# Kernel tuning notes

Measured on AMD Instinct MI355X. Metric: run time of the kernel, lower is better.

Reference implementation:

```python
import jax, jax.numpy as jnp
import numpy as np

NUM_CLASSES = 13
HIDDEN = 64
NUM_LAYERS = 2
NODE_FEAT = 1 + 4 + NUM_CLASSES  # 18
N_NODES = 100000
N_EDGES = 1600000


def _glorot(key, shape):
    fan_in, fan_out = shape[0], shape[1]
    lim = (6.0 / (fan_in + fan_out)) ** 0.5
    return jax.random.uniform(key, shape, jnp.float32, -lim, lim)


def setup_inputs() -> dict:
    key = jax.random.key(0)
    ks = jax.random.split(key, 32)
    H = HIDDEN
    inp = {
        "node_features": jax.random.normal(ks[0], (N_NODES, NODE_FEAT), jnp.float32),
        "edge_index": jax.random.randint(ks[1], (2, N_EDGES), 0, N_NODES, jnp.int32),
        "edge_weights": jax.random.uniform(ks[2], (N_EDGES,), jnp.float32),
        "embed_W": _glorot(ks[3], (NODE_FEAT, H)),
        "embed_b": jnp.zeros((H,), jnp.float32),
        # stacked per-layer params, leading dim = NUM_LAYERS
        "msg_W1": jnp.stack([_glorot(ks[4 + i], (2 * H, H)) for i in range(NUM_LAYERS)]),
        "msg_b1": jnp.zeros((NUM_LAYERS, H), jnp.float32),
        "msg_W2": jnp.stack([_glorot(ks[8 + i], (H, H)) for i in range(NUM_LAYERS)]),
        "msg_b2": jnp.zeros((NUM_LAYERS, H), jnp.float32),
        "att_W1": jnp.stack([_glorot(ks[12 + i], (2 * H, H // 2)) for i in range(NUM_LAYERS)]),
        "att_b1": jnp.zeros((NUM_LAYERS, H // 2), jnp.float32),
        "att_W2": jnp.stack([_glorot(ks[16 + i], (H // 2, 1)) for i in range(NUM_LAYERS)]),
        "att_b2": jnp.zeros((NUM_LAYERS, 1), jnp.float32),
        "upd_W1": jnp.stack([_glorot(ks[20 + i], (2 * H, H)) for i in range(NUM_LAYERS)]),
        "upd_b1": jnp.zeros((NUM_LAYERS, H), jnp.float32),
        "upd_W2": jnp.stack([_glorot(ks[24 + i], (H, H)) for i in range(NUM_LAYERS)]),
        "upd_b2": jnp.zeros((NUM_LAYERS, H), jnp.float32),
        "head_W": _glorot(ks[28], (H, 1)),
        "head_b": jnp.zeros((1,), jnp.float32),
    }
    return inp


def _mlp2(x, W1, b1, W2, b2):
    return jax.nn.relu(x @ W1 + b1) @ W2 + b2


def reference(node_features, edge_index, edge_weights,
              embed_W, embed_b,
              msg_W1, msg_b1, msg_W2, msg_b2,
              att_W1, att_b1, att_W2, att_b2,
              upd_W1, upd_b1, upd_W2, upd_b2,
              head_W, head_b):
    row, col = edge_index[0], edge_index[1]
    x = jax.nn.relu(node_features @ embed_W + embed_b)  # [N, H]
    num_nodes = x.shape[0]
    for l in range(NUM_LAYERS):
        cat = jnp.concatenate([x[row], x[col]], axis=-1)  # [E, 2H]
        messages = _mlp2(cat, msg_W1[l], msg_b1[l], msg_W2[l], msg_b2[l])  # [E, H]
        att = jax.nn.sigmoid(_mlp2(cat, att_W1[l], att_b1[l], att_W2[l], att_b2[l])[:, 0])  # [E]
        fw = edge_weights * att
        messages = messages * fw[:, None]
        aggregated = jax.ops.segment_sum(messages, col, num_segments=num_nodes)  # [N, H]
        norm = jax.ops.segment_sum(fw, col, num_segments=num_nodes)
        norm = jnp.clip(norm, 1e-6, None)
        aggregated = aggregated / norm[:, None]
        x_new = _mlp2(jnp.concatenate([x, aggregated], axis=-1),
                      upd_W1[l], upd_b1[l], upd_W2[l], upd_b2[l])
        x = jax.nn.relu(x_new + x)
    series_repr = jnp.max(x, axis=0)  # [H]
    binary_logit = (series_repr @ head_W + head_b)[0]
    return binary_logit
```

## Files before the change

### kernel.cpp

```cpp
#include <hip/hip_runtime.h>
#include <hip/hip_bf16.h>
#include <math.h>

#define H 64
#define F 18
#define NPW 16
#define NBKT 1024
#define EPB 8192

typedef _Float16 f16x8 __attribute__((ext_vector_type(8)));
typedef _Float16 f16x4 __attribute__((ext_vector_type(4)));
typedef float f32x4 __attribute__((ext_vector_type(4)));

__global__ __launch_bounds__(256) void embed_kernel(
    const float* __restrict__ nf, const float* __restrict__ W,
    const float* __restrict__ b, _Float16* __restrict__ xh, int N)
{
    int n = blockIdx.x * 256 + threadIdx.x;
    if (n >= N) return;
    float acc[H];
#pragma unroll
    for (int j = 0; j < H; ++j) acc[j] = b[j];
    const float* f = nf + (long)n * F;
#pragma unroll
    for (int i = 0; i < F; ++i) {
        float c = f[i];
        const float* w = W + i * H;
#pragma unroll
        for (int j = 0; j < H; ++j) acc[j] += c * w[j];
    }
    union { uint4 v[8]; _Float16 h[64]; } O;
#pragma unroll
    for (int j = 0; j < H; ++j) O.h[j] = (_Float16)fmaxf(acc[j], 0.f);
    uint4* xo = (uint4*)(xh + (size_t)n * H);
#pragma unroll
    for (int i = 0; i < 8; ++i) xo[i] = O.v[i];
}

__global__ __launch_bounds__(256) void packfrag_uv_kernel(
    const float* __restrict__ mW1, const float* __restrict__ aW1,
    f16x8* __restrict__ uvB)
{
    int t = blockIdx.x * 256 + threadIdx.x;
    if (t >= 3072) return;
    int lane = t & 63;
    int frag = t >> 6;
    int l = frag / 24, rem = frag % 24;
    int side = rem / 12, q = rem % 12;
    int nt = q >> 1, kk = q & 1;
    int quad = lane >> 4, l15 = lane & 15;
    int col = nt * 16 + l15;
    f16x8 v;
#pragma unroll
    for (int j = 0; j < 8; ++j) {
        int k = side * 64 + kk * 32 + quad * 8 + j;
        float w = (col < 64) ? mW1[(size_t)l * 8192 + k * 64 + col]
                             : aW1[(size_t)l * 4096 + k * 32 + (col - 64)];
        v[j] = (_Float16)w;
    }
    uvB[(size_t)frag * 64 + lane] = v;
}

__global__ __launch_bounds__(256) void prep_update_kernel(
    const float* __restrict__ mW2, const float* __restrict__ mb2,
    const float* __restrict__ uW1,
    float* __restrict__ M2U, float* __restrict__ mbu)
{
    int t = blockIdx.x * 256 + threadIdx.x;
    if (t >= 2 * 64 * 64) return;
    int l = t >> 12, r = t & 4095;
    int i = r >> 6, j = r & 63;
    const float* W2 = mW2 + (size_t)l * 4096;
    const float* U1b = uW1 + (size_t)l * 8192 + 4096;
    float s = 0.f;
    for (int k = 0; k < 64; ++k) s += W2[i * 64 + k] * U1b[k * 64 + j];
    M2U[t] = s;
    if (i == 0) {
        float sb = 0.f;
        const float* b2 = mb2 + (size_t)l * 64;
        for (int k = 0; k < 64; ++k) sb += b2[k] * U1b[k * 64 + j];
        mbu[l * 64 + j] = sb;
    }
}

__global__ __launch_bounds__(256) void packfrag_upd_kernel(
    const float* __restrict__ uW1, const float* __restrict__ M2U,
    const float* __restrict__ uW2, f16x8* __restrict__ updB)
{
    int t = blockIdx.x * 256 + threadIdx.x;
    if (t >= 3072) return;
    int lane = t & 63;
    int frag = t >> 6;
    int l = frag / 24, f = frag % 24;
    int quad = lane >> 4, l15 = lane & 15;
    int g = f >> 3, ff = f & 7;
    int nt = ff >> 1, kk = ff & 1;
    const float* src;
    if (g == 0)      src = uW1 + (size_t)l * 8192;
    else if (g == 1) src = M2U + (size_t)l * 4096;
    else             src = uW2 + (size_t)l * 4096;
    f16x8 v;
#pragma unroll
    for (int j = 0; j < 8; ++j) {
        int k = kk * 32 + quad * 8 + j;
        v[j] = (_Float16)src[k * 64 + nt * 16 + l15];
    }
    updB[(size_t)frag * 64 + lane] = v;
}

__global__ __launch_bounds__(256) void scan1_kernel(
    const int* __restrict__ deg, int* __restrict__ part,
    int* __restrict__ bsum, int N)
{
    __shared__ int lds[256];
    int t = threadIdx.x;
    int base = blockIdx.x * 1024 + t * 4;
    int v[4];
#pragma unroll
    for (int s = 0; s < 4; ++s) v[s] = (base + s < N) ? deg[base + s] : 0;
    int sum = v[0] + v[1] + v[2] + v[3];
    lds[t] = sum;
    __syncthreads();
    for (int off = 1; off < 256; off <<= 1) {
        int xv = (t >= off) ? lds[t - off] : 0;
        __syncthreads();
        lds[t] += xv;
        __syncthreads();
    }
    int excl = lds[t] - sum;
    if (t == 255) bsum[blockIdx.x] = lds[255];
    int p = excl;
#pragma unroll
    for (int s = 0; s < 4; ++s) {
        if (base + s < N) part[base + s] = p;
        p += v[s];
    }
}

__global__ __launch_bounds__(256) void scan2_kernel(int* __restrict__ bsum, int nb)
{
    __shared__ int lds[256];
    int t = threadIdx.x;
    int v = (t < nb) ? bsum[t] : 0;
    lds[t] = v;
    __syncthreads();
    for (int off = 1; off < 256; off <<= 1) {
        int xv = (t >= off) ? lds[t - off] : 0;
        __syncthreads();
        lds[t] += xv;
        __syncthreads();
    }
    if (t < nb) bsum[t] = lds[t] - v;
}

__global__ __launch_bounds__(256) void scan3_kernel(
    int* __restrict__ part, const int* __restrict__ bsum, int N)
{
    int i = blockIdx.x * 256 + threadIdx.x;
    if (i >= N) return;
    part[i] = part[i] + bsum[i >> 10];
}

__global__ __launch_bounds__(256) void count_bucket_kernel(
    const int* __restrict__ col, int* __restrict__ cnt,
    int E, int NB, int NBK, int BS)
{
    __shared__ int lc[NBKT];
    int t = threadIdx.x;
    for (int i = t; i < NBK; i += 256) lc[i] = 0;
    __syncthreads();
    for (int s = 0; s < EPB / 256; ++s) {
        int e = blockIdx.x * EPB + s * 256 + t;
        if (e < E) atomicAdd(lc + (unsigned)col[e] / (unsigned)BS, 1);
    }
    __syncthreads();
    for (int i = t; i < NBK; i += 256)
        cnt[(size_t)i * NB + blockIdx.x] = lc[i];
}

__global__ __launch_bounds__(256) void place_kernel(
    const int* __restrict__ row, const int* __restrict__ col,
    const float* __restrict__ ew, const int* __restrict__ off,
    int2* __restrict__ edata, int E, int NB, int NBK, int BS)
{
    __shared__ int lc[NBKT];
    int t = threadIdx.x;
    for (int i = t; i < NBK; i += 256) lc[i] = 0;
    __syncthreads();
    for (int s = 0; s < EPB / 256; ++s) {
        int e = blockIdx.x * EPB + s * 256 + t;
        if (e < E) {
            int cv = col[e];
            int c = (unsigned)cv / (unsigned)BS;
            int lcol = cv - c * BS;
            int r = atomicAdd(lc + c, 1);
            int pos = off[(size_t)c * NB + blockIdx.x] + r;
            edata[pos] = make_int2(row[e] | (lcol << 20), __float_as_int(ew[e]));
        }
    }
}

__global__ __launch_bounds__(256) void bucket_sort_kernel(
    int2* __restrict__ edata, const int* __restrict__ off,
    int* __restrict__ deg, int* __restrict__ startp,
    int NB, int BS, int N, int E, int NBK)
{
    __shared__ int hist[256];
    __shared__ int psum[256];
    int b = blockIdx.x;
    int t = threadIdx.x;
    int base = off[(size_t)b * NB];
    int end  = (b + 1 < NBK) ? off[(size_t)(b + 1) * NB] : E;
    int cnt = end - base;
    int nlo = b * BS;

    hist[t] = 0;
    __syncthreads();

    int2 regs[8];
    int lnode[8];
#pragma unroll
    for (int ii = 0; ii < 8; ++ii) {
        int i = t + ii * 256;
        if (i < cnt) {
            regs[ii] = edata[base + i];
            lnode[ii] = ((unsigned)regs[ii].x) >> 20;
            atomicAdd(hist + lnode[ii], 1);
        }
    }
    __syncthreads();

    int cv = hist[t];
    psum[t] = cv;
    __syncthreads();
    for (int o = 1; o < 256; o <<= 1) {
        int xv = (t >= o) ? psum[t - o] : 0;
        __syncthreads();
        psum[t] += xv;
        __syncthreads();
    }
    int excl = psum[t] - cv;
    int ng = nlo + t;
    if (t < BS && ng < N) {
        deg[ng] = cv;
        startp[ng] = base + excl;
    }
    hist[t] = excl;
    __syncthreads();

#pragma unroll
    for (int ii = 0; ii < 8; ++ii) {
        int i = t + ii * 256;
        if (i < cnt) {
            int pos = atomicAdd(hist + lnode[ii], 1);
            edata[base + pos] = make_int2(regs[ii].x & 0xFFFFF, regs[ii].y);
        }
    }
}

__global__ __launch_bounds__(256) void uv_mfma_kernel(
    const _Float16* __restrict__ xh, const f16x8* __restrict__ Bf,
    const float* __restrict__ mb1, const float* __restrict__ ab1,
    _Float16* __restrict__ UV, int N, int nbside)
{
    int bid = blockIdx.x;
    int side = (bid >= nbside) ? 1 : 0;
    int b = bid - side * nbside;
    int lane = threadIdx.x & 63;
    int wid = (b * 256 + (int)threadIdx.x) >> 6;
    int quad = lane >> 4, l15 = lane & 15;
    int nbase = wid * 64;
    if (nbase >= N) return;

    const f16x8* Bs = Bf + side * 12 * 64;
    f16x8 B[12];
#pragma unroll
    for (int i = 0; i < 12; ++i) B[i] = Bs[i * 64 + lane];
    float bv[6];
#pragma unroll
    for (int nt = 0; nt < 6; ++nt) {
        int col = nt * 16 + l15;
        bv[nt] = side ? 0.f : (col < 64 ? mb1[col] : ab1[col - 64]);
    }

    for (int mt = 0; mt < 4; ++mt) {
        int na = nbase + mt * 16 + l15;
        if (na >= N) na = N - 1;
        const f16x8* xrow = (const f16x8*)(xh + (size_t)na * H);
        f16x8 Ax[2];
        Ax[0] = xrow[quad];
        Ax[1] = xrow[4 + quad];

        f32x4 C[6];
#pragma unroll
        for (int nt = 0; nt < 6; ++nt) {
            f32x4 cc = {bv[nt], bv[nt], bv[nt], bv[nt]};
#pragma unroll
            for (int kk = 0; kk < 2; ++kk)
                cc = __builtin_amdgcn_mfma_f32_16x16x32_f16(Ax[kk], B[nt * 2 + kk], cc, 0, 0, 0);
            C[nt] = cc;
        }
#pragma unroll
        for (int r = 0; r < 4; ++r) {
            int n = nbase + mt * 16 + quad * 4 + r;
            if (n < N) {
#pragma unroll
                for (int nt = 0; nt < 6; ++nt)
                    UV[(size_t)n * 192 + side * 96 + nt * 16 + l15] = (_Float16)C[nt][r];
            }
        }
    }
}

__global__ __launch_bounds__(256) void edge_gather_kernel(
    const _Float16* __restrict__ UV,
    const int2* __restrict__ edata,
    const int* __restrict__ startp, const int* __restrict__ deg,
    const float* __restrict__ aW2, const float* __restrict__ ab2,
    _Float16* __restrict__ aggN, float* __restrict__ snorm, int N)
{
    int wid = (blockIdx.x * 256 + threadIdx.x) >> 6;
    int lane = threadIdx.x & 63;
    int g = lane >> 3, s = lane & 7;
    int n0 = wid * NPW;
    if (n0 >= N) return;
    int n1 = n0 + NPW; if (n1 > N) n1 = N;

    float aw2v[4];
#pragma unroll
    for (int j = 0; j < 4; ++j) aw2v[j] = aW2[s * 4 + j];
    float ab2v = ab2[0];

    for (int n = n0; n < n1; ++n) {
        int e0 = startp[n];
        int d = deg[n];
        int iters = (d + 7) >> 3;
        const _Float16* vrow = UV + (size_t)n * 192 + 96;
        f16x8 vm = *(const f16x8*)(vrow + s * 8);
        f16x4 va = *(const f16x4*)(vrow + 64 + s * 4);

        float acc[8];
#pragma unroll
        for (int j = 0; j < 8; ++j) acc[j] = 0.f;
        float rfw = 0.f;

        if (iters > 0) {
            int2 ed0, ed1 = {0, 0}, ed2 = {0, 0};
            f16x8 um0;
            f16x4 ua0;
            {
                int ei = g;
                ed0 = edata[e0 + (ei < d ? ei : 0)];
                const _Float16* ur = UV + (size_t)ed0.x * 192;
                um0 = *(const f16x8*)(ur + s * 8);
                ua0 = *(const f16x4*)(ur + 64 + s * 4);
            }
            if (iters > 1) {
                int ei = 8 + g;
                ed1 = edata[e0 + (ei < d ? ei : 0)];
            }
            for (int it = 0; it < iters; ++it) {
                f16x8 umn = um0;
                f16x4 uan = ua0;
                if (it + 1 < iters) {
                    const _Float16* ur = UV + (size_t)ed1.x * 192;
                    umn = *(const f16x8*)(ur + s * 8);
                    uan = *(const f16x4*)(ur + 64 + s * 4);
                }
                if (it + 2 < iters) {
                    int ei = (it + 2) * 8 + g;
                    ed2 = edata[e0 + (ei < d ? ei : 0)];
                }

                int ei = it * 8 + g;
                float ew = (ei < d) ? __int_as_float(ed0.y) : 0.f;
                float pp = 0.f;
#pragma unroll
                for (int j = 0; j < 4; ++j) {
                    _Float16 za = ua0[j] + va[j];
                    za = za > (_Float16)0 ? za : (_Float16)0;
                    pp += (float)za * aw2v[j];
                }
                pp += __shfl_xor(pp, 1);
                pp += __shfl_xor(pp, 2);
                pp += __shfl_xor(pp, 4);
                float fw = ew / (1.f + __expf(-(pp + ab2v)));
#pragma unroll
                for (int j = 0; j < 8; ++j) {
                    _Float16 z = um0[j] + vm[j];
                    z = z > (_Float16)0 ? z : (_Float16)0;
                    acc[j] += (float)z * fw;
                }
                rfw += fw;

                ed0 = ed1; ed1 = ed2; um0 = umn; ua0 = uan;
            }
        }

#pragma unroll
        for (int o = 8; o <= 32; o <<= 1) {
#pragma unroll
            for (int j = 0; j < 8; ++j) acc[j] += __shfl_xor(acc[j], o);
            rfw += __shfl_xor(rfw, o);
        }
        float inv = 1.f / fmaxf(rfw, 1e-6f);
        if (g == 0) {
            union { _Float16 h[8]; uint4 v; } O;
#pragma unroll
            for (int j = 0; j < 8; ++j) O.h[j] = (_Float16)(acc[j] * inv);
            *(uint4*)(aggN + (size_t)n * H + s * 8) = O.v;
        }
        if (lane == 0) snorm[n] = rfw * inv;
    }
}

__global__ __launch_bounds__(256, 2) void update_mfma_kernel(
    _Float16* __restrict__ xh, const _Float16* __restrict__ agg,
    const float* __restrict__ snorm,
    const f16x8* __restrict__ Bfrag,
    const float* __restrict__ mbu,
    const float* __restrict__ ub1, const float* __restrict__ ub2, int N)
{
    __shared__ __align__(16) _Float16 hlds[4][16 * 80];
    int wib = threadIdx.x >> 6;
    int lane = threadIdx.x & 63;
    int wid = (blockIdx.x * 256 + threadIdx.x) >> 6;
    int quad = lane >> 4, l15 = lane & 15;
    int nbase = wid * 64;
    if (nbase >= N) return;

    f16x8 Bu[8], Bm[8], Bw[8];
#pragma unroll
    for (int i = 0; i < 8; ++i) {
        Bu[i] = Bfrag[i * 64 + lane];
        Bm[i] = Bfrag[(8 + i) * 64 + lane];
        Bw[i] = Bfrag[(16 + i) * 64 + lane];
    }
    float mbuv[4], b1v[4], b2v[4];
#pragma unroll
    for (int nt = 0; nt < 4; ++nt) {
        mbuv[nt] = mbu[nt * 16 + l15];
        b1v[nt] = ub1[nt * 16 + l15];
        b2v[nt] = ub2[nt * 16 + l15];
    }

    for (int mt = 0; mt < 4; ++mt) {
        int na = nbase + mt * 16 + l15;
        if (na >= N) na = N - 1;
        const f16x8* xrow = (const f16x8*)(xh + (size_t)na * H);
        f16x8 Ax[2];
        Ax[0] = xrow[quad];
        Ax[1] = xrow[4 + quad];
        const f16x8* arow = (const f16x8*)(agg + (size_t)na * H);
        f16x8 Aa[2];
        Aa[0] = arow[quad];
        Aa[1] = arow[4 + quad];

        f32x4 Cx[4], Ca[4];
#pragma unroll
        for (int nt = 0; nt < 4; ++nt) {
            f32x4 cx = {0.f, 0.f, 0.f, 0.f}, ca = {0.f, 0.f, 0.f, 0.f};
#pragma unroll
            for (int kk = 0; kk < 2; ++kk) {
                cx = __builtin_amdgcn_mfma_f32_16x16x32_f16(Ax[kk], Bu[nt * 2 + kk], cx, 0, 0, 0);
                ca = __builtin_amdgcn_mfma_f32_16x16x32_f16(Aa[kk], Bm[nt * 2 + kk], ca, 0, 0, 0);
            }
            Cx[nt] = cx; Ca[nt] = ca;
        }

        int noder = nbase + mt * 16 + quad * 4;
        float sn_r[4];
#pragma unroll
        for (int r = 0; r < 4; ++r) {
            int ng = noder + r; if (ng >= N) ng = N - 1;
            sn_r[r] = snorm[ng];
        }

#pragma unroll
        for (int nt = 0; nt < 4; ++nt) {
#pragma unroll
            for (int r = 0; r < 4; ++r) {
                float hv = fmaxf(Cx[nt][r] + Ca[nt][r]
                                 + sn_r[r] * mbuv[nt] + b1v[nt], 0.f);
                hlds[wib][(quad * 4 + r) * 80 + nt * 16 + l15] = (_Float16)hv;
            }
        }
        __asm__ __volatile__("s_waitcnt lgkmcnt(0)" ::: "memory");
        f16x8 Ah[2];
        Ah[0] = *(const f16x8*)&hlds[wib][l15 * 80 + quad * 8];
        Ah[1] = *(const f16x8*)&hlds[wib][l15 * 80 + 32 + quad * 8];
        __asm__ __volatile__("s_waitcnt lgkmcnt(0)" ::: "memory");

        f32x4 C2[4];
#pragma unroll
        for (int nt = 0; nt < 4; ++nt) {
            f32x4 cc = {0.f, 0.f, 0.f, 0.f};
#pragma unroll
            for (int kk = 0; kk < 2; ++kk)
                cc = __builtin_amdgcn_mfma_f32_16x16x32_f16(Ah[kk], Bw[nt * 2 + kk], cc, 0, 0, 0);
            C2[nt] = cc;
        }

#pragma unroll
        for (int r = 0; r < 4; ++r) {
            int ng = noder + r;
            if (ng < N) {
#pragma unroll
                for (int nt = 0; nt < 4; ++nt) {
                    size_t idx = (size_t)ng * H + nt * 16 + l15;
                    float xo = (float)xh[idx];
                    xh[idx] = (_Float16)fmaxf(C2[nt][r] + b2v[nt] + xo, 0.f);
                }
            }
        }
    }
}

__global__ __launch_bounds__(256) void max_kernel(
    const _Float16* __restrict__ xh16, unsigned int* __restrict__ serp, int N)
{
    int j = threadIdx.x & (H - 1);
    int g = (blockIdx.x * 256 + threadIdx.x) >> 6;
    int stride = (gridDim.x * 256) >> 6;
    float m = 0.f;
    for (int n = g; n < N; n += stride)
        m = fmaxf(m, (float)xh16[(size_t)n * H + j]);
    atomicMax(serp + j, __float_as_uint(m));
}

__global__ void head_kernel(const unsigned int* __restrict__ serp,
                            const float* __restrict__ hW,
                            const float* __restrict__ hb,
                            float* __restrict__ out)
{
    int j = threadIdx.x;
    float v = __uint_as_float(serp[j]) * hW[j];
#pragma unroll
    for (int off = 32; off > 0; off >>= 1) v += __shfl_down(v, off);
    if (j == 0) out[0] = v + hb[0];
}

extern "C" void kernel_launch(void* const* d_in, const int* in_sizes, int n_in,
                              void* d_out, int out_size, void* d_ws, size_t ws_size,
                              hipStream_t stream)
{
    const float* nf  = (const float*)d_in[0];
    const int*   ei  = (const int*)d_in[1];
    const float* ew  = (const float*)d_in[2];
    const float* eW  = (const float*)d_in[3];
    const float* eb_ = (const float*)d_in[4];
    const float* mW1 = (const float*)d_in[5];
    const float* mb1 = (const float*)d_in[6];
    const float* mW2 = (const float*)d_in[7];
    const float* mb2 = (const float*)d_in[8];
    const float* aW1 = (const float*)d_in[9];
    const float* ab1 = (const float*)d_in[10];
    const float* aW2 = (const float*)d_in[11];
    const float* ab2 = (const float*)d_in[12];
    const float* uW1 = (const float*)d_in[13];
    const float* ub1 = (const float*)d_in[14];
    const float* uW2 = (const float*)d_in[15];
    const float* ub2 = (const float*)d_in[16];
    const float* hW  = (const float*)d_in[17];
    const float* hb  = (const float*)d_in[18];

    int N = in_sizes[0] / F;
    int E = in_sizes[2];
    const int* row = ei;
    const int* col = ei + E;

    size_t Nr = ((size_t)N + 3) & ~(size_t)3;
    size_t Er = ((size_t)E + 3) & ~(size_t)3;

    int BS  = (N + NBKT - 1) / NBKT;
    int NBK = (N + BS - 1) / BS;
    int NB  = (E + EPB - 1) / EPB;
    size_t M  = (size_t)NBK * NB;
    size_t Mr = (M + 3) & ~(size_t)3;

    _Float16* xh   = (_Float16*)d_ws;
    _Float16* aggN = xh + Nr * 64;
    float* snorm   = (float*)(aggN + Nr * 64);
    unsigned int* serp = (unsigned int*)(snorm + Nr);
    int* deg       = (int*)(serp + 64);
    int* startp    = deg + Nr;
    int* bsum      = startp + Nr;
    float* M2U     = (float*)(bsum + 256);
    float* mbu     = M2U + 8192;
    f16x8* updB    = (f16x8*)(mbu + 128);
    f16x8* uvB     = updB + 3072;
    _Float16* UV   = (_Float16*)(uvB + 3072);
    int* cnt       = (int*)(UV + Nr * 192);
    int* off       = cnt + Mr;
    int2* edata    = (int2*)(off + Mr);

    int nb_n = (N + 255) / 256;
    int nbA = (int)((M + 1023) / 1024);

    count_bucket_kernel<<<NB, 256, 0, stream>>>(col, cnt, E, NB, NBK, BS);
    scan1_kernel<<<nbA, 256, 0, stream>>>(cnt, off, bsum, (int)M);
    scan2_kernel<<<1, 256, 0, stream>>>(bsum, nbA);
    scan3_kernel<<<(int)((M + 255) / 256), 256, 0, stream>>>(off, bsum, (int)M);
    place_kernel<<<NB, 256, 0, stream>>>(row, col, ew, off, edata, E, NB, NBK, BS);
    bucket_sort_kernel<<<NBK, 256, 0, stream>>>(edata, off, deg, startp,
                                                NB, BS, N, E, NBK);

    packfrag_uv_kernel<<<12, 256, 0, stream>>>(mW1, aW1, uvB);
    prep_update_kernel<<<32, 256, 0, stream>>>(mW2, mb2, uW1, M2U, mbu);
    packfrag_upd_kernel<<<12, 256, 0, stream>>>(uW1, M2U, uW2, updB);
    embed_kernel<<<nb_n, 256, 0, stream>>>(nf, eW, eb_, xh, N);

    int nwaves_n = (N + 63) / 64;
    int nb_uv = (N + 255) / 256;
    int nb_eg = (N + NPW * 4 - 1) / (NPW * 4);
    for (int l = 0; l < 2; ++l) {
        uv_mfma_kernel<<<2 * nb_uv, 256, 0, stream>>>(
            xh, uvB + (size_t)l * 24 * 64,
            mb1 + (size_t)l * H, ab1 + (size_t)l * (H / 2), UV, N, nb_uv);
        edge_gather_kernel<<<nb_eg, 256, 0, stream>>>(
            UV, edata, startp, deg,
            aW2 + (size_t)l * (H / 2), ab2 + (size_t)l,
            aggN, snorm, N);
        update_mfma_kernel<<<(nwaves_n + 3) / 4, 256, 0, stream>>>(
            xh, aggN, snorm,
            updB + (size_t)l * 24 * 64,
            mbu + (size_t)l * 64,
            ub1 + (size_t)l * H, ub2 + (size_t)l * H, N);
    }

    hipMemsetAsync(serp, 0, 64 * sizeof(unsigned int), stream);
    max_kernel<<<256, 256, 0, stream>>>(xh, serp, N);
    head_kernel<<<1, 64, 0, stream>>>(serp, hW, hb, (float*)d_out);
}
```

Baseline: 420.9 us.

## Fuse next-layer UV projection and final max into update kernel, shrink NPW

The layer-0 update kernel now also computes the layer-1 UV projection from the freshly updated node rows held in registers. This removes the separate uv_mfma launch and the re-read of xh for layer 1. The layer-1 update kernel now does the column-wise max reduction with atomics, so the standalone max kernel is gone. NPW drops from 16 to 4, which launches more edge-gather blocks. The fused update kernel carries more registers and weight loads, which may lower occupancy.

```diff
diff --git a/kernel.cpp b/kernel.cpp
--- a/kernel.cpp
+++ b/kernel.cpp
@@ -4,7 +4,7 @@
 
 #define H 64
 #define F 18
-#define NPW 16
+#define NPW 4
 #define NBKT 1024
 #define EPB 8192
 
@@ -419,7 +419,12 @@
     const float* __restrict__ snorm,
     const f16x8* __restrict__ Bfrag,
     const float* __restrict__ mbu,
-    const float* __restrict__ ub1, const float* __restrict__ ub2, int N)
+    const float* __restrict__ ub1, const float* __restrict__ ub2,
+    const f16x8* __restrict__ uvBn,
+    const float* __restrict__ mb1n, const float* __restrict__ ab1n,
+    _Float16* __restrict__ UV,
+    unsigned int* __restrict__ serp,
+    int N, int doMax)
 {
     __shared__ __align__(16) _Float16 hlds[4][16 * 80];
     int wib = threadIdx.x >> 6;
@@ -443,6 +448,16 @@
         b1v[nt] = ub1[nt * 16 + l15];
         b2v[nt] = ub2[nt * 16 + l15];
     }
+    float bvn[12];
+    if (uvBn) {
+#pragma unroll
+        for (int q = 0; q < 12; ++q) {
+            int sd = q / 6, nt2 = q % 6;
+            int col = nt2 * 16 + l15;
+            bvn[q] = sd ? 0.f : (col < 64 ? mb1n[col] : ab1n[col - 64]);
+        }
+    }
+    float lmax[4] = {0.f, 0.f, 0.f, 0.f};
 
     for (int mt = 0; mt < 4; ++mt) {
         int na = nbase + mt * 16 + l15;
@@ -501,6 +516,7 @@
             C2[nt] = cc;
         }
 
+        float xn[4][4];
 #pragma unroll
         for (int r = 0; r < 4; ++r) {
             int ng = noder + r;
@@ -509,23 +525,61 @@
                 for (int nt = 0; nt < 4; ++nt) {
                     size_t idx = (size_t)ng * H + nt * 16 + l15;
                     float xo = (float)xh[idx];
-                    xh[idx] = (_Float16)fmaxf(C2[nt][r] + b2v[nt] + xo, 0.f);
+                    float v = fmaxf(C2[nt][r] + b2v[nt] + xo, 0.f);
+                    xn[nt][r] = v;
+                    xh[idx] = (_Float16)v;
                 }
-            }
-        }
-    }
-}
-
-__global__ __launch_bounds__(256) void max_kernel(
-    const _Float16* __restrict__ xh16, unsigned int* __restrict__ serp, int N)
-{
-    int j = threadIdx.x & (H - 1);
-    int g = (blockIdx.x * 256 + threadIdx.x) >> 6;
-    int stride = (gridDim.x * 256) >> 6;
-    float m = 0.f;
-    for (int n = g; n < N; n += stride)
-        m = fmaxf(m, (float)xh16[(size_t)n * H + j]);
-    atomicMax(serp + j, __float_as_uint(m));
+            } else {
+#pragma unroll
+                for (int nt = 0; nt < 4; ++nt) xn[nt][r] = 0.f;
+            }
+        }
+        if (doMax) {
+#pragma unroll
+            for (int nt = 0; nt < 4; ++nt)
+#pragma unroll
+                for (int r = 0; r < 4; ++r) lmax[nt] = fmaxf(lmax[nt], xn[nt][r]);
+        }
+
+        if (uvBn) {
+#pragma unroll
+            for (int nt = 0; nt < 4; ++nt)
+#pragma unroll
+                for (int r = 0; r < 4; ++r)
+                    hlds[wib][(quad * 4 + r) * 80 + nt * 16 + l15] = (_Float16)xn[nt][r];
+            __asm__ __volatile__("s_waitcnt lgkmcnt(0)" ::: "memory");
+            f16x8 A2[2];
+            A2[0] = *(const f16x8*)&hlds[wib][l15 * 80 + quad * 8];
+            A2[1] = *(const f16x8*)&hlds[wib][l15 * 80 + 32 + quad * 8];
+            __asm__ __volatile__("s_waitcnt lgkmcnt(0)" ::: "memory");
+
+#pragma unroll
+            for (int q = 0; q < 12; ++q) {
+                int sd = q / 6, nt2 = q % 6;
+                f16x8 Ba = uvBn[(sd * 12 + nt2 * 2) * 64 + lane];
+                f16x8 Bb = uvBn[(sd * 12 + nt2 * 2 + 1) * 64 + lane];
+                f32x4 cc = {bvn[q], bvn[q], bvn[q], bvn[q]};
+                cc = __builtin_amdgcn_mfma_f32_16x16x32_f16(A2[0], Ba, cc, 0, 0, 0);
+                cc = __builtin_amdgcn_mfma_f32_16x16x32_f16(A2[1], Bb, cc, 0, 0, 0);
+#pragma unroll
+                for (int r = 0; r < 4; ++r) {
+                    int n = noder + r;
+                    if (n < N)
+                        UV[(size_t)n * 192 + sd * 96 + nt2 * 16 + l15] = (_Float16)cc[r];
+                }
+            }
+        }
+    }
+
+    if (doMax) {
+#pragma unroll
+        for (int nt = 0; nt < 4; ++nt) {
+            float m = lmax[nt];
+            m = fmaxf(m, __shfl_xor(m, 16));
+            m = fmaxf(m, __shfl_xor(m, 32));
+            if (quad == 0) atomicMax(serp + nt * 16 + l15, __float_as_uint(m));
+        }
+    }
 }
 
 __global__ void head_kernel(const unsigned int* __restrict__ serp,
@@ -597,6 +651,7 @@
     int nb_n = (N + 255) / 256;
     int nbA = (int)((M + 1023) / 1024);
 
+    hipMemsetAsync(serp, 0, 64 * sizeof(unsigned int), stream);
     count_bucket_kernel<<<NB, 256, 0, stream>>>(col, cnt, E, NB, NBK, BS);
     scan1_kernel<<<nbA, 256, 0, stream>>>(cnt, off, bsum, (int)M);
     scan2_kernel<<<1, 256, 0, stream>>>(bsum, nbA);
@@ -613,22 +668,20 @@
     int nwaves_n = (N + 63) / 64;
     int nb_uv = (N + 255) / 256;
     int nb_eg = (N + NPW * 4 - 1) / (NPW * 4);
-    for (int l = 0; l < 2; ++l) {
-        uv_mfma_kernel<<<2 * nb_uv, 256, 0, stream>>>(
-            xh, uvB + (size_t)l * 24 * 64,
-            mb1 + (size_t)l * H, ab1 + (size_t)l * (H / 2), UV, N, nb_uv);
-        edge_gather_kernel<<<nb_eg, 256, 0, stream>>>(
-            UV, edata, startp, deg,
-            aW2 + (size_t)l * (H / 2), ab2 + (size_t)l,
-            aggN, snorm, N);
-        update_mfma_kernel<<<(nwaves_n + 3) / 4, 256, 0, stream>>>(
-            xh, aggN, snorm,
-            updB + (size_t)l * 24 * 64,
-            mbu + (size_t)l * 64,
-            ub1 + (size_t)l * H, ub2 + (size_t)l * H, N);
-    }
-
-    hipMemsetAsync(serp, 0, 64 * sizeof(unsigned int), stream);
-    max_kernel<<<256, 256, 0, stream>>>(xh, serp, N);
+    int nb_up = (nwaves_n + 3) / 4;
+
+    uv_mfma_kernel<<<2 * nb_uv, 256, 0, stream>>>(
+        xh, uvB, mb1, ab1, UV, N, nb_uv);
+    edge_gather_kernel<<<nb_eg, 256, 0, stream>>>(
+        UV, edata, startp, deg, aW2, ab2, aggN, snorm, N);
+    update_mfma_kernel<<<nb_up, 256, 0, stream>>>(
+        xh, aggN, snorm, updB, mbu, ub1, ub2,
+        uvB + 24 * 64, mb1 + H, ab1 + (H / 2), UV, nullptr, N, 0);
+    edge_gather_kernel<<<nb_eg, 256, 0, stream>>>(
+        UV, edata, startp, deg, aW2 + (H / 2), ab2 + 1, aggN, snorm, N);
+    update_mfma_kernel<<<nb_up, 256, 0, stream>>>(
+        xh, aggN, snorm, updB + 24 * 64, mbu + 64, ub1 + H, ub2 + H,
+        nullptr, nullptr, nullptr, nullptr, serp, N, 1);
+
     head_kernel<<<1, 64, 0, stream>>>(serp, hW, hb, (float*)d_out);
 }
```

New measurement: 392.4 us. 1.07x faster.
